# Optimization experiments

Hardware: AMD Instinct MI355X
Metric: run time of the kernel (lower is better)

## Reference

```python
import jax, jax.numpy as jnp
import numpy as np

DIM = 512
NUM_HEADS = 8
HEAD_DIM = DIM // NUM_HEADS        # 64
L_HEADS = 4                        # int(8 * 0.5)
H_HEADS = NUM_HEADS - L_HEADS      # 4
L_DIM = L_HEADS * HEAD_DIM         # 256
H_DIM = H_HEADS * HEAD_DIM         # 256
WS = 2                             # window_size
SCALE = HEAD_DIM ** -0.5
SEQ_LEN = 1024


def setup_inputs() -> dict:
    key = jax.random.key(0)
    ks = jax.random.split(key, 13)
    B, N, C = 16, 1024, DIM
    def w(k, shape, fan_in):
        return (jax.random.normal(k, shape, jnp.float32) / np.sqrt(fan_in)).astype(jnp.float32)
    return {
        "x": jax.random.normal(ks[0], (B, N, C), jnp.float32),
        "pos_emb": jax.random.normal(ks[1], (1, SEQ_LEN, C), jnp.float32) * 0.02,
        "l_q_w": w(ks[2], (C, L_DIM), C),
        "l_kv_w": w(ks[3], (C, 2 * L_DIM), C),
        "l_proj_w": w(ks[4], (L_DIM, L_DIM), L_DIM),
        "l_proj_b": jax.random.normal(ks[5], (L_DIM,), jnp.float32) * 0.01,
        "h_qkv_w": w(ks[6], (C, 3 * H_DIM), C),
        "h_proj_w": w(ks[7], (H_DIM, H_DIM), H_DIM),
        "h_proj_b": jax.random.normal(ks[8], (H_DIM,), jnp.float32) * 0.01,
        "in_proj_w": w(ks[9], (C, 3 * C), C),
        "in_proj_b": jax.random.normal(ks[10], (3 * C,), jnp.float32) * 0.01,
        "out_proj_w": w(ks[11], (C, C), C),
        "out_proj_b": jax.random.normal(ks[12], (C,), jnp.float32) * 0.01,
        "H": 32,
        "W": 32,
    }


def _hifi(xg, h_qkv_w, h_proj_w, h_proj_b, H, W):
    B, _, _, C = xg.shape
    hg, wg = H // WS, W // WS
    G, T = hg * wg, WS * WS
    # [B, hg, WS, wg, WS, C] -> [B, G, T, C] (window partition)
    xw = xg.reshape(B, hg, WS, wg, WS, C).transpose(0, 1, 3, 2, 4, 5).reshape(B, G, T, C)
    qkv = (xw @ h_qkv_w).reshape(B, G, T, 3, H_HEADS, HEAD_DIM)
    q = qkv[:, :, :, 0].transpose(0, 1, 3, 2, 4)  # [B,G,h,T,d]
    k = qkv[:, :, :, 1].transpose(0, 1, 3, 2, 4)
    v = qkv[:, :, :, 2].transpose(0, 1, 3, 2, 4)
    attn = jax.nn.softmax(jnp.einsum("bghtd,bghsd->bghts", q, k) * SCALE, axis=-1)
    o = jnp.einsum("bghts,bghsd->bghtd", attn, v)
    # window un-partition: [B,G,h,T,d] -> [B,H,W,h_dim]
    o = o.transpose(0, 1, 3, 2, 4).reshape(B, hg, wg, WS, WS, H_DIM)
    o = o.transpose(0, 1, 3, 2, 4, 5).reshape(B, H, W, H_DIM)
    return o @ h_proj_w + h_proj_b


def _lofi(xg, l_q_w, l_kv_w, l_proj_w, l_proj_b, H, W):
    B, _, _, C = xg.shape
    N = H * W
    q = (xg @ l_q_w).reshape(B, N, L_HEADS, HEAD_DIM)
    kv = (xg @ l_kv_w).reshape(B, N, 2, L_HEADS, HEAD_DIM)
    k, v = kv[:, :, 0], kv[:, :, 1]
    attn = jax.nn.softmax(jnp.einsum("bnhd,bmhd->bhnm", q, k) * SCALE, axis=-1)
    o = jnp.einsum("bhnm,bmhd->bnhd", attn, v).reshape(B, H, W, L_DIM)
    return o @ l_proj_w + l_proj_b


def _mha(y, in_proj_w, in_proj_b, out_proj_w, out_proj_b):
    B, N, C = y.shape
    qkv = y @ in_proj_w + in_proj_b
    q, k, v = jnp.split(qkv, 3, axis=-1)
    q = q.reshape(B, N, NUM_HEADS, HEAD_DIM)
    k = k.reshape(B, N, NUM_HEADS, HEAD_DIM)
    v = v.reshape(B, N, NUM_HEADS, HEAD_DIM)
    attn = jax.nn.softmax(jnp.einsum("bnhd,bmhd->bhnm", q, k) * SCALE, axis=-1)
    o = jnp.einsum("bhnm,bmhd->bnhd", attn, v).reshape(B, N, C)
    return o @ out_proj_w + out_proj_b


def reference(x, pos_emb, l_q_w, l_kv_w, l_proj_w, l_proj_b,
              h_qkv_w, h_proj_w, h_proj_b,
              in_proj_w, in_proj_b, out_proj_w, out_proj_b, H, W):
    B, N, C = x.shape
    x = x + pos_emb[:, :N, :]
    xg = x.reshape(B, H, W, C)
    hifi_out = _hifi(xg, h_qkv_w, h_proj_w, h_proj_b, H, W)
    lofi_out = _lofi(xg, l_q_w, l_kv_w, l_proj_w, l_proj_b, H, W)
    y = jnp.concatenate([hifi_out, lofi_out], axis=-1).reshape(B, N, C)
    return _mha(y, in_proj_w, in_proj_b, out_proj_w, out_proj_b)
```

## Files before the change

### kernel.cpp

```cpp
#include <hip/hip_runtime.h>

typedef unsigned short ushort_t;
typedef short bf16x8 __attribute__((ext_vector_type(8)));
typedef float f32x4 __attribute__((ext_vector_type(4)));

#define DEV __device__ __forceinline__

DEV ushort_t f2bf(float f) {
  return (ushort_t)((__float_as_uint(f) + 0x8000u) >> 16);
}
DEV unsigned pk_bf16(float lo, float hi) {
  unsigned a = __float_as_uint(lo) + 0x8000u;
  unsigned b = __float_as_uint(hi) + 0x8000u;
  return __builtin_amdgcn_perm(b, a, 0x07060302);
}
DEV float bf2f(ushort_t h) {
  union { unsigned int u; float f; } v; v.u = ((unsigned int)h) << 16;
  return v.f;
}
DEV f32x4 mfma16(bf16x8 a, bf16x8 b, f32x4 c) {
  return __builtin_amdgcn_mfma_f32_16x16x32_bf16(a, b, c, 0, 0, 0);
}
typedef __attribute__((address_space(3))) void lds_void;
typedef const __attribute__((address_space(1))) void glb_void;
DEV void gl_lds16(const void* g, void* l) {
  __builtin_amdgcn_global_load_lds((glb_void*)g, (lds_void*)l, 16, 0, 0);
}

__global__ __launch_bounds__(256)
void gemm_bt(const ushort_t* __restrict__ A, int lda,
             const ushort_t* __restrict__ BT,
             const float* __restrict__ bias,
             ushort_t* __restrict__ Cb, float* __restrict__ Cf,
             int ldc, int coff, int K, float scv, int sc_lo, int sc_hi)
{
  __shared__ __align__(16) ushort_t As[128 * 32];
  __shared__ __align__(16) ushort_t Bs[128 * 32];
  const int tid  = threadIdx.x;
  const int wave = tid >> 6, lane = tid & 63;
  const int quad = lane >> 4, r16 = lane & 15;
  const int m0 = blockIdx.x * 128, n0 = blockIdx.y * 128;
  const int wm = (wave >> 1) * 64, wn = (wave & 1) * 64;

  f32x4 acc[4][4];
#pragma unroll
  for (int i = 0; i < 4; ++i)
#pragma unroll
    for (int j = 0; j < 4; ++j) acc[i][j] = (f32x4){0.f, 0.f, 0.f, 0.f};

  for (int kc = 0; kc < K; kc += 32) {
#pragma unroll
    for (int p = 0; p < 4; ++p) {
      int wp = p * 4 + wave;
      int lc = ((wp & 7) << 6) + lane;
      int row = lc >> 2, e8 = (lc & 3) * 8;
      if (wp < 8) gl_lds16(&A[(size_t)(m0 + row) * lda + kc + e8], &As[lc * 8]);
      else        gl_lds16(&BT[(size_t)(n0 + row) * K  + kc + e8], &Bs[lc * 8]);
    }
    __syncthreads();
    bf16x8 af[4], bfr[4];
#pragma unroll
    for (int i = 0; i < 4; ++i) {
      af[i]  = *(const bf16x8*)&As[(wm + i * 16 + r16) * 32 + quad * 8];
      bfr[i] = *(const bf16x8*)&Bs[(wn + i * 16 + r16) * 32 + quad * 8];
    }
#pragma unroll
    for (int mi = 0; mi < 4; ++mi)
#pragma unroll
      for (int ni = 0; ni < 4; ++ni)
        acc[mi][ni] = mfma16(af[mi], bfr[ni], acc[mi][ni]);
    __syncthreads();
  }

#pragma unroll
  for (int mi = 0; mi < 4; ++mi) {
#pragma unroll
    for (int ni = 0; ni < 4; ++ni) {
      int col = n0 + wn + ni * 16 + r16;
      float bv = bias ? bias[col] : 0.f;
      float s = (col >= sc_lo && col < sc_hi) ? scv : 1.0f;
#pragma unroll
      for (int r = 0; r < 4; ++r) {
        int row = m0 + wm + mi * 16 + quad * 4 + r;
        float v = (acc[mi][ni][r] + bv) * s;
        if (Cf) Cf[(size_t)row * ldc + coff + col] = v;
        else    Cb[(size_t)row * ldc + coff + col] = f2bf(v);
      }
    }
  }
}

__global__ __launch_bounds__(256)
void flash_attn7(const ushort_t* __restrict__ Q, int qs, int q_ch,
                 const ushort_t* __restrict__ Kg, int ks, int k_ch,
                 const ushort_t* __restrict__ vT,
                 ushort_t* __restrict__ O, int os, int o_ch,
                 int N)
{
  __shared__ __align__(16) ushort_t Ks[2][64 * 64];
  __shared__ __align__(16) ushort_t Vs[2][64 * 64];

  const int H = gridDim.y;
  const int tid = threadIdx.x, wave = tid >> 6, lane = tid & 63;
  const int quad = lane >> 4, c16 = lane & 15;

  const int nwg = gridDim.x * H * gridDim.z;
  const int lin = blockIdx.x + gridDim.x * (blockIdx.y + H * blockIdx.z);
  const int logical = (lin & 7) * (nwg >> 3) + (lin >> 3);
  const int qb = logical & 7;
  const int t8 = logical >> 3;
  const int b = (H == 8) ? (t8 >> 3) : (t8 >> 2);
  const int h = t8 - b * H;
  const int q0 = qb * 128 + wave * 32;

  bf16x8 qf[2][2];
#pragma unroll
  for (int qt = 0; qt < 2; ++qt) {
    const ushort_t* qp = Q + ((size_t)b * N + q0 + qt * 16 + c16) * qs + q_ch + h * 64;
    qf[qt][0] = *(const bf16x8*)&qp[quad * 8];
    qf[qt][1] = *(const bf16x8*)&qp[32 + quad * 8];
  }
  const ushort_t* kbase = Kg + ((size_t)b * N) * ks + k_ch + h * 64;
  const ushort_t* vbase = vT + ((size_t)(b * H + h) * 64) * N;

  f32x4 oacc[2][4];
#pragma unroll
  for (int qt = 0; qt < 2; ++qt)
#pragma unroll
    for (int dt = 0; dt < 4; ++dt) oacc[qt][dt] = (f32x4){0.f, 0.f, 0.f, 0.f};
  float l_acc[2] = {0.f, 0.f};

  const int laneA = (2 * (quad & 1)) * 16 + c16;
  const int laneB = laneA + 16;

  const int eo0 = (quad ^ (c16 & 7)) * 8;
  const int eo1 = eo0 ^ 32;

  auto stage = [&](int s0, int buf) {
#pragma unroll
    for (int p = 0; p < 4; ++p) {
      int wp = p * 4 + wave;
      int lc = ((wp & 7) << 6) + lane;
      int row = lc >> 3, c = lc & 7;
      int e8 = ((c ^ (row & 7)) * 8);
      if (wp < 8) gl_lds16(kbase + (size_t)(s0 + row) * ks + e8, &Ks[buf][lc * 8]);
      else        gl_lds16(vbase + (size_t)row * N + s0 + e8,    &Vs[buf][lc * 8]);
    }
  };

  stage(0, 0);
  const int NT = N >> 6;
  for (int it = 0; it < NT; ++it) {
    const int cur = it & 1;
    __syncthreads();
    if (it + 1 < NT) stage((it + 1) << 6, cur ^ 1);

    f32x4 st[4][2];
#pragma unroll
    for (int si = 0; si < 4; ++si) {
      const ushort_t* kr = &Ks[cur][(si * 16 + c16) * 64];
      bf16x8 kf0 = *(const bf16x8*)&kr[eo0];
      bf16x8 kf1 = *(const bf16x8*)&kr[eo1];
#pragma unroll
      for (int qt = 0; qt < 2; ++qt) {
        f32x4 z = (f32x4){0.f, 0.f, 0.f, 0.f};
        z = mfma16(kf0, qf[qt][0], z);
        z = mfma16(kf1, qf[qt][1], z);
        st[si][qt] = z;
      }
    }

    bf16x8 pA[2], pB[2];
#pragma unroll
    for (int qt = 0; qt < 2; ++qt) {
      float tsum = 0.f;
      unsigned pks[4][2];
#pragma unroll
      for (int si = 0; si < 4; ++si) {
        float p0 = __builtin_amdgcn_exp2f(st[si][qt][0]);
        float p1 = __builtin_amdgcn_exp2f(st[si][qt][1]);
        float p2 = __builtin_amdgcn_exp2f(st[si][qt][2]);
        float p3 = __builtin_amdgcn_exp2f(st[si][qt][3]);
        tsum += (p0 + p1) + (p2 + p3);
        pks[si][0] = pk_bf16(p0, p1);
        pks[si][1] = pk_bf16(p2, p3);
      }
      l_acc[qt] += tsum;

      union U8 { bf16x8 f; unsigned u[4]; } pf0, pf1;
      const bool hiq = quad >= 2;
#pragma unroll
      for (int i = 0; i < 4; ++i) {
        int src = (i < 2) ? laneA : laneB;
        unsigned a0 = __shfl(pks[0][i & 1], src);
        unsigned a1 = __shfl(pks[1][i & 1], src);
        unsigned a2 = __shfl(pks[2][i & 1], src);
        unsigned a3 = __shfl(pks[3][i & 1], src);
        pf0.u[i] = hiq ? a1 : a0;
        pf1.u[i] = hiq ? a3 : a2;
      }
      pA[qt] = pf0.f;
      pB[qt] = pf1.f;
    }

#pragma unroll
    for (int dt = 0; dt < 4; ++dt) {
      const ushort_t* vr = &Vs[cur][(dt * 16 + c16) * 64];
      bf16x8 vf0 = *(const bf16x8*)&vr[eo0];
      bf16x8 vf1 = *(const bf16x8*)&vr[eo1];
#pragma unroll
      for (int qt = 0; qt < 2; ++qt) {
        oacc[qt][dt] = mfma16(vf0, pA[qt], oacc[qt][dt]);
        oacc[qt][dt] = mfma16(vf1, pB[qt], oacc[qt][dt]);
      }
    }
  }

#pragma unroll
  for (int qt = 0; qt < 2; ++qt) {
    float l = l_acc[qt];
    l += __shfl_xor(l, 16);
    l += __shfl_xor(l, 32);
    float inv = 1.f / l;
    ushort_t* op = O + ((size_t)b * N + q0 + qt * 16 + c16) * os + o_ch + h * 64;
#pragma unroll
    for (int dt = 0; dt < 4; ++dt) {
      uint2 pkv;
      pkv.x = pk_bf16(oacc[qt][dt][0] * inv, oacc[qt][dt][1] * inv);
      pkv.y = pk_bf16(oacc[qt][dt][2] * inv, oacc[qt][dt][3] * inv);
      *(uint2*)&op[dt * 16 + quad * 4] = pkv;
    }
  }
}

__global__ __launch_bounds__(256)
void transpose_v(const ushort_t* __restrict__ in, int ld, int ch,
                 ushort_t* __restrict__ out, int N, int H)
{
  __shared__ __align__(16) ushort_t T[64][72];
  const int s0 = blockIdx.x * 64, h = blockIdx.y, b = blockIdx.z;
  const int tid = threadIdx.x;
#pragma unroll
  for (int p = 0; p < 2; ++p) {
    int c = p * 256 + tid;
    int sr = c >> 3, d0 = (c & 7) * 8;
    *(uint4*)&T[sr][d0] =
        *(const uint4*)&in[((size_t)b * N + s0 + sr) * ld + ch + h * 64 + d0];
  }
  __syncthreads();
  const int d = tid >> 2, sp = (tid & 3) * 16;
  union { uint4 v; ushort_t u[8]; } A, B;
#pragma unroll
  for (int j = 0; j < 8; ++j) { A.u[j] = T[sp + j][d]; B.u[j] = T[sp + 8 + j][d]; }
  ushort_t* op = out + ((size_t)(b * H + h) * 64 + d) * N + s0 + sp;
  *(uint4*)&op[0] = A.v;
  *(uint4*)&op[8] = B.v;
}

__global__ __launch_bounds__(256)
void hifi_win(const ushort_t* __restrict__ qkv, int ld, ushort_t* __restrict__ out)
{
  const int bg = blockIdx.x;
  const int b = bg >> 8, g = bg & 255;
  const int head = threadIdx.x >> 6, lane = threadIdx.x & 63;
  const int gh = g >> 4, gw = g & 15;

  int n[4];
  float q[4], k[4], v[4];
#pragma unroll
  for (int t = 0; t < 4; ++t) {
    n[t] = (gh * 2 + (t >> 1)) * 32 + gw * 2 + (t & 1);
    size_t base = ((size_t)b * 1024 + n[t]) * ld + head * 64 + lane;
    q[t] = bf2f(qkv[base]);
    k[t] = bf2f(qkv[base + 256]);
    v[t] = bf2f(qkv[base + 512]);
  }
  float sc[4][4];
#pragma unroll
  for (int t = 0; t < 4; ++t)
#pragma unroll
    for (int s = 0; s < 4; ++s) {
      float p = q[t] * k[s];
#pragma unroll
      for (int off = 32; off >= 1; off >>= 1) p += __shfl_xor(p, off);
      sc[t][s] = p * 0.125f;
    }
#pragma unroll
  for (int t = 0; t < 4; ++t) {
    float m = fmaxf(fmaxf(sc[t][0], sc[t][1]), fmaxf(sc[t][2], sc[t][3]));
    float p0 = __expf(sc[t][0] - m), p1 = __expf(sc[t][1] - m);
    float p2 = __expf(sc[t][2] - m), p3 = __expf(sc[t][3] - m);
    float sum = p0 + p1 + p2 + p3;
    float o = (p0 * v[0] + p1 * v[1] + p2 * v[2] + p3 * v[3]) / sum;
    out[((size_t)b * 1024 + n[t]) * 512 + head * 64 + lane] = f2bf(o);
  }
}

struct WEnt { const float* W; ushort_t* WT; int K; int N; };
struct WArgs { WEnt e[7]; };

__global__ __launch_bounds__(256)
void w_prep(WArgs a)
{
  WEnt w = a.e[blockIdx.z];
  if ((int)blockIdx.x >= (w.K >> 6) || (int)blockIdx.y >= (w.N >> 6)) return;
  __shared__ float T[64][65];
  const int k0 = blockIdx.x * 64, n0 = blockIdx.y * 64;
  const int tid = threadIdx.x;
#pragma unroll
  for (int p = 0; p < 4; ++p) {
    int c = p * 256 + tid;
    int kr = c >> 4, f4 = (c & 15) * 4;
    float4 v = *(const float4*)&w.W[(size_t)(k0 + kr) * w.N + n0 + f4];
    T[f4 + 0][kr] = v.x; T[f4 + 1][kr] = v.y;
    T[f4 + 2][kr] = v.z; T[f4 + 3][kr] = v.w;
  }
  __syncthreads();
  const int nl = tid >> 2, kp = (tid & 3) * 16;
  union { uint4 v; ushort_t u[8]; } A, B;
#pragma unroll
  for (int j = 0; j < 8; ++j) {
    A.u[j] = f2bf(T[nl][kp + j]);
    B.u[j] = f2bf(T[nl][kp + 8 + j]);
  }
  ushort_t* op = w.WT + (size_t)(n0 + nl) * w.K + k0 + kp;
  *(uint4*)&op[0] = A.v;
  *(uint4*)&op[8] = B.v;
}

__global__ void add_pos(const float* __restrict__ x, const float* __restrict__ pos,
                        ushort_t* __restrict__ xpe)
{
  int idx = blockIdx.x * 256 + threadIdx.x;
  int e = idx * 4;
  float4 xv = *(const float4*)&x[e];
  float4 pv = *(const float4*)&pos[e & (512 * 1024 - 1)];
  uint2 pk;
  pk.x = pk_bf16(xv.x + pv.x, xv.y + pv.y);
  pk.y = pk_bf16(xv.z + pv.z, xv.w + pv.w);
  *(uint2*)&xpe[e] = pk;
}

extern "C" void kernel_launch(void* const* d_in, const int* in_sizes, int n_in,
                              void* d_out, int out_size, void* d_ws, size_t ws_size,
                              hipStream_t stream)
{
  const float* x         = (const float*)d_in[0];
  const float* pos       = (const float*)d_in[1];
  const float* l_q_w     = (const float*)d_in[2];
  const float* l_kv_w    = (const float*)d_in[3];
  const float* l_proj_w  = (const float*)d_in[4];
  const float* l_proj_b  = (const float*)d_in[5];
  const float* h_qkv_w   = (const float*)d_in[6];
  const float* h_proj_w  = (const float*)d_in[7];
  const float* h_proj_b  = (const float*)d_in[8];
  const float* in_proj_w = (const float*)d_in[9];
  const float* in_proj_b = (const float*)d_in[10];
  const float* out_proj_w= (const float*)d_in[11];
  const float* out_proj_b= (const float*)d_in[12];
  float* out = (float*)d_out;

  const float QSCALE = 0.125f * 1.44269504f;

  char* ws = (char*)d_ws;
  ushort_t* xpe = (ushort_t*)(ws);
  ushort_t* y   = (ushort_t*)(ws + (size_t)16777216);
  ushort_t* F   = (ushort_t*)(ws + (size_t)33554432);
  ushort_t* rB  = (ushort_t*)(ws + (size_t)83886080);
  ushort_t* wb  = (ushort_t*)(ws + (size_t)100663296);

  ushort_t* F_T      = wb;
  ushort_t* h_projT  = wb + 786432;
  ushort_t* l_projT  = wb + 851968;
  ushort_t* in_projT = wb + 917504;
  ushort_t* out_projT= wb + 1703936;

  const int M = 16384;
  ushort_t* vT_lo = xpe;
  ushort_t* vT_m  = rB;

  WArgs wa;
  wa.e[0] = {h_qkv_w,   F_T,                 512, 768};
  wa.e[1] = {l_q_w,     F_T + 768 * 512,     512, 256};
  wa.e[2] = {l_kv_w,    F_T + 1024 * 512,    512, 512};
  wa.e[3] = {h_proj_w,  h_projT,             256, 256};
  wa.e[4] = {l_proj_w,  l_projT,             256, 256};
  wa.e[5] = {in_proj_w, in_projT,            512, 1536};
  wa.e[6] = {out_proj_w,out_projT,           512, 512};
  w_prep<<<dim3(8, 24, 7), dim3(256), 0, stream>>>(wa);

  add_pos<<<dim3(8192), dim3(256), 0, stream>>>(x, pos, xpe);

  gemm_bt<<<dim3(M / 128, 12), dim3(256), 0, stream>>>(
      xpe, 512, F_T, nullptr, F, nullptr, 1536, 0, 512, QSCALE, 768, 1024);
  hifi_win<<<dim3(4096), dim3(256), 0, stream>>>(F, 1536, rB);
  transpose_v<<<dim3(16, 4, 16), dim3(256), 0, stream>>>(
      F, 1536, 1280, vT_lo, 1024, 4);
  flash_attn7<<<dim3(8, 4, 16), dim3(256), 0, stream>>>(
      F, 1536, 768, F, 1536, 1024, vT_lo, rB, 512, 256, 1024);
  gemm_bt<<<dim3(M / 128, 2), dim3(256), 0, stream>>>(
      rB, 512, h_projT, h_proj_b, y, nullptr, 512, 0, 256, 1.0f, 0, 0);
  gemm_bt<<<dim3(M / 128, 2), dim3(256), 0, stream>>>(
      rB + 256, 512, l_projT, l_proj_b, y, nullptr, 512, 256, 256, 1.0f, 0, 0);
  gemm_bt<<<dim3(M / 128, 12), dim3(256), 0, stream>>>(
      y, 512, in_projT, in_proj_b, F, nullptr, 1536, 0, 512, QSCALE, 0, 512);
  transpose_v<<<dim3(16, 8, 16), dim3(256), 0, stream>>>(
      F, 1536, 1024, vT_m, 1024, 8);
  flash_attn7<<<dim3(8, 8, 16), dim3(256), 0, stream>>>(
      F, 1536, 0, F, 1536, 512, vT_m, xpe, 512, 0, 1024);
  gemm_bt<<<dim3(M / 128, 4), dim3(256), 0, stream>>>(
      xpe, 512, out_projT, out_proj_b, nullptr, out, 512, 0, 512, 1.0f, 0, 0);
}
```

Before: 363.3 us.

## Add 256x256-tile 8-wave GEMM with interleaved prefetch for QKV projections

Adds a new GEMM kernel that uses 256x256 output tiles with 512 threads, double-buffered LDS staging whose next-tile loads are interleaved between MFMA phases, s_setprio around the MFMA bursts, and an XCD-aware block remapping. The two large QKV projection GEMMs (N=1536) switch from the 128-tile gemm_bt to this kernel to raise operand reuse and overlap loads with compute. The cost is higher register and LDS use (128 KB LDS per block, 32 accumulators per lane) and fewer blocks in flight, which can limit occupancy.

```diff
diff --git a/kernel.cpp b/kernel.cpp
--- a/kernel.cpp
+++ b/kernel.cpp
@@ -83,6 +83,155 @@
       for (int r = 0; r < 4; ++r) {
         int row = m0 + wm + mi * 16 + quad * 4 + r;
         float v = (acc[mi][ni][r] + bv) * s;
+        if (Cf) Cf[(size_t)row * ldc + coff + col] = v;
+        else    Cb[(size_t)row * ldc + coff + col] = f2bf(v);
+      }
+    }
+  }
+}
+
+__global__ __launch_bounds__(512, 2)
+void gemm256(const ushort_t* __restrict__ A, int lda,
+             const ushort_t* __restrict__ BT,
+             const float* __restrict__ bias,
+             ushort_t* __restrict__ Cb, float* __restrict__ Cf,
+             int ldc, int coff, int K, float scv, int sc_lo, int sc_hi,
+             int nbn)
+{
+  __shared__ __align__(16) ushort_t Ab[2][256 * 64];
+  __shared__ __align__(16) ushort_t Bb[2][256 * 64];
+
+  const int tid  = threadIdx.x;
+  const int wave = tid >> 6, lane = tid & 63;
+  const int quad = lane >> 4, r16 = lane & 15;
+  const int wm = wave >> 2, wn = wave & 3;
+
+  const int nwg = gridDim.x;
+  const int lin = blockIdx.x;
+  const int logical = (lin & 7) * (nwg >> 3) + (lin >> 3);
+  const int mb = logical / nbn, nb = logical - mb * nbn;
+  const int m0 = mb * 256, n0 = nb * 256;
+
+  f32x4 acc[8][4];
+#pragma unroll
+  for (int i = 0; i < 8; ++i)
+#pragma unroll
+    for (int j = 0; j < 4; ++j) acc[i][j] = (f32x4){0.f, 0.f, 0.f, 0.f};
+
+  auto stageA = [&](int t, int slot) {
+#pragma unroll
+    for (int l = 0; l < 4; ++l) {
+      int c = l * 512 + tid;
+      int row = c >> 3, cc = c & 7;
+      int sc = cc ^ (row & 7);
+      gl_lds16(&A[(size_t)(m0 + row) * lda + t * 64 + sc * 8],
+               &Ab[slot][c * 8]);
+    }
+  };
+  auto stageB = [&](int t, int slot) {
+#pragma unroll
+    for (int l = 0; l < 4; ++l) {
+      int c = l * 512 + tid;
+      int row = c >> 3, cc = c & 7;
+      int sc = cc ^ (row & 7);
+      gl_lds16(&BT[(size_t)(n0 + row) * K + t * 64 + sc * 8],
+               &Bb[slot][c * 8]);
+    }
+  };
+  auto ldaf = [&](int slot, int row, int kk) -> bf16x8 {
+    int ch = ((kk << 2) + quad) ^ (row & 7);
+    return *(const bf16x8*)&Ab[slot][row * 64 + ch * 8];
+  };
+  auto ldbf = [&](int slot, int row, int kk) -> bf16x8 {
+    int ch = ((kk << 2) + quad) ^ (row & 7);
+    return *(const bf16x8*)&Bb[slot][row * 64 + ch * 8];
+  };
+
+  stageA(0, 0);
+  stageB(0, 0);
+  __syncthreads();
+
+  const int NT = K >> 6;
+  bf16x8 bfr[4];
+  for (int t = 0; t < NT; ++t) {
+    const int cur = t & 1;
+    const bool pre = (t + 1 < NT);
+
+    {
+      bf16x8 af[4];
+#pragma unroll
+      for (int i = 0; i < 4; ++i) af[i] = ldaf(cur, wm * 128 + i * 16 + r16, 0);
+#pragma unroll
+      for (int j = 0; j < 4; ++j) bfr[j] = ldbf(cur, wn * 64 + j * 16 + r16, 0);
+      if (pre) stageA(t + 1, cur ^ 1);
+      __builtin_amdgcn_s_barrier();
+      __builtin_amdgcn_s_setprio(1);
+#pragma unroll
+      for (int i = 0; i < 4; ++i)
+#pragma unroll
+        for (int j = 0; j < 4; ++j)
+          acc[i][j] = mfma16(af[i], bfr[j], acc[i][j]);
+      __builtin_amdgcn_s_setprio(0);
+      __builtin_amdgcn_s_barrier();
+    }
+    {
+      bf16x8 af[4];
+#pragma unroll
+      for (int i = 0; i < 4; ++i) af[i] = ldaf(cur, wm * 128 + (4 + i) * 16 + r16, 0);
+      if (pre) stageB(t + 1, cur ^ 1);
+      __builtin_amdgcn_s_barrier();
+      __builtin_amdgcn_s_setprio(1);
+#pragma unroll
+      for (int i = 0; i < 4; ++i)
+#pragma unroll
+        for (int j = 0; j < 4; ++j)
+          acc[4 + i][j] = mfma16(af[i], bfr[j], acc[4 + i][j]);
+      __builtin_amdgcn_s_setprio(0);
+      __builtin_amdgcn_s_barrier();
+    }
+    {
+      bf16x8 af[4];
+#pragma unroll
+      for (int i = 0; i < 4; ++i) af[i] = ldaf(cur, wm * 128 + i * 16 + r16, 1);
+#pragma unroll
+      for (int j = 0; j < 4; ++j) bfr[j] = ldbf(cur, wn * 64 + j * 16 + r16, 1);
+      __builtin_amdgcn_s_barrier();
+      __builtin_amdgcn_s_setprio(1);
+#pragma unroll
+      for (int i = 0; i < 4; ++i)
+#pragma unroll
+        for (int j = 0; j < 4; ++j)
+          acc[i][j] = mfma16(af[i], bfr[j], acc[i][j]);
+      __builtin_amdgcn_s_setprio(0);
+      __builtin_amdgcn_s_barrier();
+    }
+    {
+      bf16x8 af[4];
+#pragma unroll
+      for (int i = 0; i < 4; ++i) af[i] = ldaf(cur, wm * 128 + (4 + i) * 16 + r16, 1);
+      __builtin_amdgcn_s_barrier();
+      __builtin_amdgcn_s_setprio(1);
+#pragma unroll
+      for (int i = 0; i < 4; ++i)
+#pragma unroll
+        for (int j = 0; j < 4; ++j)
+          acc[4 + i][j] = mfma16(af[i], bfr[j], acc[4 + i][j]);
+      __builtin_amdgcn_s_setprio(0);
+    }
+    __syncthreads();
+  }
+
+#pragma unroll
+  for (int mi = 0; mi < 8; ++mi) {
+#pragma unroll
+    for (int nj = 0; nj < 4; ++nj) {
+      int col = n0 + wn * 64 + nj * 16 + r16;
+      float bv = bias ? bias[col] : 0.f;
+      float s = (col >= sc_lo && col < sc_hi) ? scv : 1.0f;
+#pragma unroll
+      for (int r = 0; r < 4; ++r) {
+        int row = m0 + wm * 128 + mi * 16 + quad * 4 + r;
+        float v = (acc[mi][nj][r] + bv) * s;
         if (Cf) Cf[(size_t)row * ldc + coff + col] = v;
         else    Cb[(size_t)row * ldc + coff + col] = f2bf(v);
       }
@@ -391,8 +540,8 @@
 
   add_pos<<<dim3(8192), dim3(256), 0, stream>>>(x, pos, xpe);
 
-  gemm_bt<<<dim3(M / 128, 12), dim3(256), 0, stream>>>(
-      xpe, 512, F_T, nullptr, F, nullptr, 1536, 0, 512, QSCALE, 768, 1024);
+  gemm256<<<dim3((M / 256) * 6), dim3(512), 0, stream>>>(
+      xpe, 512, F_T, nullptr, F, nullptr, 1536, 0, 512, QSCALE, 768, 1024, 6);
   hifi_win<<<dim3(4096), dim3(256), 0, stream>>>(F, 1536, rB);
   transpose_v<<<dim3(16, 4, 16), dim3(256), 0, stream>>>(
       F, 1536, 1280, vT_lo, 1024, 4);
@@ -402,8 +551,8 @@
       rB, 512, h_projT, h_proj_b, y, nullptr, 512, 0, 256, 1.0f, 0, 0);
   gemm_bt<<<dim3(M / 128, 2), dim3(256), 0, stream>>>(
       rB + 256, 512, l_projT, l_proj_b, y, nullptr, 512, 256, 256, 1.0f, 0, 0);
-  gemm_bt<<<dim3(M / 128, 12), dim3(256), 0, stream>>>(
-      y, 512, in_projT, in_proj_b, F, nullptr, 1536, 0, 512, QSCALE, 0, 512);
+  gemm256<<<dim3((M / 256) * 6), dim3(512), 0, stream>>>(
+      y, 512, in_projT, in_proj_b, F, nullptr, 1536, 0, 512, QSCALE, 0, 512, 6);
   transpose_v<<<dim3(16, 8, 16), dim3(256), 0, stream>>>(
       F, 1536, 1024, vT_m, 1024, 8);
   flash_attn7<<<dim3(8, 8, 16), dim3(256), 0, stream>>>(
```

Measured after the change: 371.6 us. 1.02x slower.

## Switch flash attention to 32x32x16 MFMA with permlane32 swap for P relayout

Applied to the files above, without the earlier changes.

Rewrites the attention inner loop to use 32x32x16 bf16 MFMA tiles instead of 16x16x32, so each wave handles 32 queries against 32-key blocks with fewer instructions and fewer LDS fragment loads. The softmax probabilities are repacked into the B-operand layout with v_permlane32_swap instead of many __shfl calls and selects. The risks are larger accumulator register pressure (two f32x16 accumulators plus a 16-wide score tile) and the need for the new fragment indexing and output layout to match exactly. The unnormalized exp2 softmax without max subtraction from before is kept.

```diff
diff --git a/kernel.cpp b/kernel.cpp
--- a/kernel.cpp
+++ b/kernel.cpp
@@ -3,6 +3,7 @@
 typedef unsigned short ushort_t;
 typedef short bf16x8 __attribute__((ext_vector_type(8)));
 typedef float f32x4 __attribute__((ext_vector_type(4)));
+typedef float f32x16 __attribute__((ext_vector_type(16)));
 
 #define DEV __device__ __forceinline__
 
@@ -20,6 +21,12 @@
 }
 DEV f32x4 mfma16(bf16x8 a, bf16x8 b, f32x4 c) {
   return __builtin_amdgcn_mfma_f32_16x16x32_bf16(a, b, c, 0, 0, 0);
+}
+DEV f32x16 mfma32(bf16x8 a, bf16x8 b, f32x16 c) {
+  return __builtin_amdgcn_mfma_f32_32x32x16_bf16(a, b, c, 0, 0, 0);
+}
+DEV void pl32swap(unsigned &a, unsigned &b) {
+  asm("v_permlane32_swap_b32 %0, %1" : "+v"(a), "+v"(b));
 }
 typedef __attribute__((address_space(3))) void lds_void;
 typedef const __attribute__((address_space(1))) void glb_void;
@@ -91,7 +98,7 @@
 }
 
 __global__ __launch_bounds__(256)
-void flash_attn7(const ushort_t* __restrict__ Q, int qs, int q_ch,
+void flash_attn8(const ushort_t* __restrict__ Q, int qs, int q_ch,
                  const ushort_t* __restrict__ Kg, int ks, int k_ch,
                  const ushort_t* __restrict__ vT,
                  ushort_t* __restrict__ O, int os, int o_ch,
@@ -102,7 +109,7 @@
 
   const int H = gridDim.y;
   const int tid = threadIdx.x, wave = tid >> 6, lane = tid & 63;
-  const int quad = lane >> 4, c16 = lane & 15;
+  const int c = lane & 31, hh = lane >> 5;
 
   const int nwg = gridDim.x * H * gridDim.z;
   const int lin = blockIdx.x + gridDim.x * (blockIdx.y + H * blockIdx.z);
@@ -113,36 +120,27 @@
   const int h = t8 - b * H;
   const int q0 = qb * 128 + wave * 32;
 
-  bf16x8 qf[2][2];
-#pragma unroll
-  for (int qt = 0; qt < 2; ++qt) {
-    const ushort_t* qp = Q + ((size_t)b * N + q0 + qt * 16 + c16) * qs + q_ch + h * 64;
-    qf[qt][0] = *(const bf16x8*)&qp[quad * 8];
-    qf[qt][1] = *(const bf16x8*)&qp[32 + quad * 8];
+  bf16x8 qf[4];
+  {
+    const ushort_t* qp = Q + ((size_t)b * N + q0 + c) * qs + q_ch + h * 64 + hh * 8;
+#pragma unroll
+    for (int s = 0; s < 4; ++s) qf[s] = *(const bf16x8*)&qp[s * 16];
   }
   const ushort_t* kbase = Kg + ((size_t)b * N) * ks + k_ch + h * 64;
   const ushort_t* vbase = vT + ((size_t)(b * H + h) * 64) * N;
 
-  f32x4 oacc[2][4];
-#pragma unroll
-  for (int qt = 0; qt < 2; ++qt)
-#pragma unroll
-    for (int dt = 0; dt < 4; ++dt) oacc[qt][dt] = (f32x4){0.f, 0.f, 0.f, 0.f};
-  float l_acc[2] = {0.f, 0.f};
-
-  const int laneA = (2 * (quad & 1)) * 16 + c16;
-  const int laneB = laneA + 16;
-
-  const int eo0 = (quad ^ (c16 & 7)) * 8;
-  const int eo1 = eo0 ^ 32;
+  f32x16 oacc[2];
+#pragma unroll
+  for (int i = 0; i < 16; ++i) { oacc[0][i] = 0.f; oacc[1][i] = 0.f; }
+  float l_acc = 0.f;
 
   auto stage = [&](int s0, int buf) {
 #pragma unroll
     for (int p = 0; p < 4; ++p) {
       int wp = p * 4 + wave;
       int lc = ((wp & 7) << 6) + lane;
-      int row = lc >> 3, c = lc & 7;
-      int e8 = ((c ^ (row & 7)) * 8);
+      int row = lc >> 3, cc = lc & 7;
+      int e8 = ((cc ^ (row & 7)) * 8);
       if (wp < 8) gl_lds16(kbase + (size_t)(s0 + row) * ks + e8, &Ks[buf][lc * 8]);
       else        gl_lds16(vbase + (size_t)row * N + s0 + e8,    &Vs[buf][lc * 8]);
     }
@@ -155,80 +153,63 @@
     __syncthreads();
     if (it + 1 < NT) stage((it + 1) << 6, cur ^ 1);
 
-    f32x4 st[4][2];
-#pragma unroll
-    for (int si = 0; si < 4; ++si) {
-      const ushort_t* kr = &Ks[cur][(si * 16 + c16) * 64];
-      bf16x8 kf0 = *(const bf16x8*)&kr[eo0];
-      bf16x8 kf1 = *(const bf16x8*)&kr[eo1];
-#pragma unroll
-      for (int qt = 0; qt < 2; ++qt) {
-        f32x4 z = (f32x4){0.f, 0.f, 0.f, 0.f};
-        z = mfma16(kf0, qf[qt][0], z);
-        z = mfma16(kf1, qf[qt][1], z);
-        st[si][qt] = z;
+    bf16x8 Bf[4];
+#pragma unroll
+    for (int kb = 0; kb < 2; ++kb) {
+      f32x16 z;
+#pragma unroll
+      for (int i = 0; i < 16; ++i) z[i] = 0.f;
+      const int krow = kb * 32 + c;
+      const ushort_t* kr = &Ks[cur][krow * 64];
+#pragma unroll
+      for (int s = 0; s < 4; ++s) {
+        bf16x8 kf = *(const bf16x8*)&kr[(((s << 1) + hh) ^ (krow & 7)) * 8];
+        z = mfma32(kf, qf[s], z);
       }
-    }
-
-    bf16x8 pA[2], pB[2];
-#pragma unroll
-    for (int qt = 0; qt < 2; ++qt) {
-      float tsum = 0.f;
-      unsigned pks[4][2];
-#pragma unroll
-      for (int si = 0; si < 4; ++si) {
-        float p0 = __builtin_amdgcn_exp2f(st[si][qt][0]);
-        float p1 = __builtin_amdgcn_exp2f(st[si][qt][1]);
-        float p2 = __builtin_amdgcn_exp2f(st[si][qt][2]);
-        float p3 = __builtin_amdgcn_exp2f(st[si][qt][3]);
-        tsum += (p0 + p1) + (p2 + p3);
-        pks[si][0] = pk_bf16(p0, p1);
-        pks[si][1] = pk_bf16(p2, p3);
+      float ts = 0.f;
+      unsigned W[8];
+#pragma unroll
+      for (int t = 0; t < 8; ++t) {
+        float p0 = __builtin_amdgcn_exp2f(z[2 * t]);
+        float p1 = __builtin_amdgcn_exp2f(z[2 * t + 1]);
+        ts += p0 + p1;
+        W[t] = pk_bf16(p0, p1);
       }
-      l_acc[qt] += tsum;
-
-      union U8 { bf16x8 f; unsigned u[4]; } pf0, pf1;
-      const bool hiq = quad >= 2;
-#pragma unroll
-      for (int i = 0; i < 4; ++i) {
-        int src = (i < 2) ? laneA : laneB;
-        unsigned a0 = __shfl(pks[0][i & 1], src);
-        unsigned a1 = __shfl(pks[1][i & 1], src);
-        unsigned a2 = __shfl(pks[2][i & 1], src);
-        unsigned a3 = __shfl(pks[3][i & 1], src);
-        pf0.u[i] = hiq ? a1 : a0;
-        pf1.u[i] = hiq ? a3 : a2;
+      l_acc += ts;
+      union U8 { bf16x8 f; unsigned u[4]; } f0, f1;
+      unsigned a0 = W[0], b0 = W[2]; pl32swap(a0, b0);
+      unsigned a1 = W[1], b1 = W[3]; pl32swap(a1, b1);
+      f0.u[0] = a0; f0.u[1] = a1; f0.u[2] = b0; f0.u[3] = b1;
+      unsigned a2 = W[4], b2 = W[6]; pl32swap(a2, b2);
+      unsigned a3 = W[5], b3 = W[7]; pl32swap(a3, b3);
+      f1.u[0] = a2; f1.u[1] = a3; f1.u[2] = b2; f1.u[3] = b3;
+      Bf[kb * 2]     = f0.f;
+      Bf[kb * 2 + 1] = f1.f;
+    }
+
+#pragma unroll
+    for (int db = 0; db < 2; ++db) {
+      const int vrow = db * 32 + c;
+      const ushort_t* vr = &Vs[cur][vrow * 64];
+#pragma unroll
+      for (int s = 0; s < 4; ++s) {
+        bf16x8 vf = *(const bf16x8*)&vr[(((s << 1) + hh) ^ (vrow & 7)) * 8];
+        oacc[db] = mfma32(vf, Bf[s], oacc[db]);
       }
-      pA[qt] = pf0.f;
-      pB[qt] = pf1.f;
-    }
-
-#pragma unroll
-    for (int dt = 0; dt < 4; ++dt) {
-      const ushort_t* vr = &Vs[cur][(dt * 16 + c16) * 64];
-      bf16x8 vf0 = *(const bf16x8*)&vr[eo0];
-      bf16x8 vf1 = *(const bf16x8*)&vr[eo1];
-#pragma unroll
-      for (int qt = 0; qt < 2; ++qt) {
-        oacc[qt][dt] = mfma16(vf0, pA[qt], oacc[qt][dt]);
-        oacc[qt][dt] = mfma16(vf1, pB[qt], oacc[qt][dt]);
-      }
-    }
-  }
-
-#pragma unroll
-  for (int qt = 0; qt < 2; ++qt) {
-    float l = l_acc[qt];
-    l += __shfl_xor(l, 16);
-    l += __shfl_xor(l, 32);
-    float inv = 1.f / l;
-    ushort_t* op = O + ((size_t)b * N + q0 + qt * 16 + c16) * os + o_ch + h * 64;
-#pragma unroll
-    for (int dt = 0; dt < 4; ++dt) {
+    }
+  }
+
+  float l = l_acc + __shfl_xor(l_acc, 32);
+  float inv = 1.f / l;
+  ushort_t* op = O + ((size_t)b * N + q0 + c) * os + o_ch + h * 64;
+#pragma unroll
+  for (int db = 0; db < 2; ++db) {
+#pragma unroll
+    for (int g = 0; g < 4; ++g) {
       uint2 pkv;
-      pkv.x = pk_bf16(oacc[qt][dt][0] * inv, oacc[qt][dt][1] * inv);
-      pkv.y = pk_bf16(oacc[qt][dt][2] * inv, oacc[qt][dt][3] * inv);
-      *(uint2*)&op[dt * 16 + quad * 4] = pkv;
+      pkv.x = pk_bf16(oacc[db][4 * g + 0] * inv, oacc[db][4 * g + 1] * inv);
+      pkv.y = pk_bf16(oacc[db][4 * g + 2] * inv, oacc[db][4 * g + 3] * inv);
+      *(uint2*)&op[db * 32 + g * 8 + hh * 4] = pkv;
     }
   }
 }
@@ -396,7 +377,7 @@
   hifi_win<<<dim3(4096), dim3(256), 0, stream>>>(F, 1536, rB);
   transpose_v<<<dim3(16, 4, 16), dim3(256), 0, stream>>>(
       F, 1536, 1280, vT_lo, 1024, 4);
-  flash_attn7<<<dim3(8, 4, 16), dim3(256), 0, stream>>>(
+  flash_attn8<<<dim3(8, 4, 16), dim3(256), 0, stream>>>(
       F, 1536, 768, F, 1536, 1024, vT_lo, rB, 512, 256, 1024);
   gemm_bt<<<dim3(M / 128, 2), dim3(256), 0, stream>>>(
       rB, 512, h_projT, h_proj_b, y, nullptr, 512, 0, 256, 1.0f, 0, 0);
@@ -406,7 +387,7 @@
       y, 512, in_projT, in_proj_b, F, nullptr, 1536, 0, 512, QSCALE, 0, 512);
   transpose_v<<<dim3(16, 8, 16), dim3(256), 0, stream>>>(
       F, 1536, 1024, vT_m, 1024, 8);
-  flash_attn7<<<dim3(8, 8, 16), dim3(256), 0, stream>>>(
+  flash_attn8<<<dim3(8, 8, 16), dim3(256), 0, stream>>>(
       F, 1536, 0, F, 1536, 512, vT_m, xpe, 512, 0, 1024);
   gemm_bt<<<dim3(M / 128, 4), dim3(256), 0, stream>>>(
       xpe, 512, out_projT, out_proj_b, nullptr, out, 512, 0, 512, 1.0f, 0, 0);
```

After: 348.7 us. 4.0% less time.
